# Kernel optimization log

Hardware: AMD Instinct MI355X
Metric: run time of the kernel (lower is better)

The kernel has to match this reference:

```python
import jax, jax.numpy as jnp
import numpy as np

EMBED = 512
HEADS = 8
HEAD_DIM = EMBED // HEADS


def setup_inputs() -> dict:
    key = jax.random.key(0)
    ks = jax.random.split(key, 8)
    N, S = 4, 2048
    values = jax.random.normal(ks[0], (N, S, EMBED), dtype=jnp.float32)
    keys = jax.random.normal(ks[1], (N, S, EMBED), dtype=jnp.float32)
    query = jax.random.normal(ks[2], (N, S, EMBED), dtype=jnp.float32)
    mask = jnp.ones((N, 1, 1, S), dtype=jnp.int32)
    # per-head projection weights (nn.Linear: y = x @ W.T), no bias
    Wv = jax.random.normal(ks[3], (HEAD_DIM, HEAD_DIM), dtype=jnp.float32) / np.sqrt(HEAD_DIM)
    Wk = jax.random.normal(ks[4], (HEAD_DIM, HEAD_DIM), dtype=jnp.float32) / np.sqrt(HEAD_DIM)
    Wq = jax.random.normal(ks[5], (HEAD_DIM, HEAD_DIM), dtype=jnp.float32) / np.sqrt(HEAD_DIM)
    Wo = jax.random.normal(ks[6], (EMBED, EMBED), dtype=jnp.float32) / np.sqrt(EMBED)
    bo = jax.random.normal(ks[7], (EMBED,), dtype=jnp.float32) * 0.01
    return {"values": values, "keys": keys, "query": query, "mask": mask,
            "Wv": Wv, "Wk": Wk, "Wq": Wq, "Wo": Wo, "bo": bo}


def reference(values, keys, query, mask, Wv, Wk, Wq, Wo, bo):
    N, S, _ = query.shape
    scale = jnp.sqrt(jnp.float32(HEAD_DIM))
    v = values.reshape(N, S, HEADS, HEAD_DIM) @ Wv.T
    k = keys.reshape(N, S, HEADS, HEAD_DIM) @ Wk.T
    q = query.reshape(N, S, HEADS, HEAD_DIM) @ Wq.T
    energy = jnp.einsum('nqhd,nkhd->nhqk', q, k) / scale  # [N,H,S,S]
    energy = jnp.where(mask == 0, jnp.float32(-1e20), energy)
    attn = jax.nn.softmax(energy, axis=3)
    # dropout is identity in eval mode
    out = jnp.einsum('nhql,nlhd->nqhd', attn, v).reshape(N, S, EMBED)
    return out @ Wo.T + bo
```

## Files before the change

kernel.cpp:

```cpp
#include <hip/hip_runtime.h>
#include <hip/hip_bf16.h>

#define EMB 512
#define NHEADS 8
#define HD 64
#define SEQ 2048

typedef float f32x4 __attribute__((ext_vector_type(4)));
typedef short short8 __attribute__((ext_vector_type(8)));
typedef unsigned short ushort4_t __attribute__((ext_vector_type(4)));

#define MFMA(a, b, c) __builtin_amdgcn_mfma_f32_16x16x32_bf16((a), (b), (c), 0, 0, 0)

__device__ inline unsigned short f2bf(float f) {
    union { float f; unsigned u; } v; v.f = f;
    unsigned r = v.u + 0x7fffu + ((v.u >> 16) & 1u);
    return (unsigned short)(r >> 16);
}

__device__ inline unsigned cvt_pk_bf16(float a, float b) {
    unsigned r;
    asm("v_cvt_pk_bf16_f32 %0, %1, %2" : "=v"(r) : "v"(a), "v"(b));
    return r;
}

__device__ inline short8 f8_to_bf8(float4 a, float4 b) {
    short8 r;
    r[0] = (short)f2bf(a.x); r[1] = (short)f2bf(a.y);
    r[2] = (short)f2bf(a.z); r[3] = (short)f2bf(a.w);
    r[4] = (short)f2bf(b.x); r[5] = (short)f2bf(b.y);
    r[6] = (short)f2bf(b.z); r[7] = (short)f2bf(b.w);
    return r;
}

__global__ __launch_bounds__(256) void qkv_proj_kernel(
    const float* __restrict__ vin, const float* __restrict__ kin,
    const float* __restrict__ qin, const unsigned short* __restrict__ wqkvb,
    unsigned short* __restrict__ q_ws, unsigned short* __restrict__ k_ws,
    unsigned short* __restrict__ vt_ws)
{
    const int z = blockIdx.y;
    const float* __restrict__ x = (z == 0) ? qin : (z == 1 ? kin : vin);
    const unsigned short* __restrict__ wb = wqkvb + z * HD * HD;

    const int bid = blockIdx.x;
    const int st = bid & 15;
    const int h  = (bid >> 4) & 7;
    const int n  = bid >> 7;

    const int lane = threadIdx.x & 63;
    const int w    = threadIdx.x >> 6;
    const int lo = lane & 15, hi = lane >> 4;
    const int s_base = st * 128 + w * 32;

    short8 b[2][4];
#pragma unroll
    for (int nb = 0; nb < 4; ++nb)
#pragma unroll
        for (int kb = 0; kb < 2; ++kb)
            b[kb][nb] = *(const short8*)(wb + (lo + 16 * nb) * HD + kb * 32 + hi * 8);

    short8 a[2][2];
#pragma unroll
    for (int sub = 0; sub < 2; ++sub) {
        const float* xr = x + ((size_t)n * SEQ + s_base + 16 * sub + lo) * EMB + h * HD;
#pragma unroll
        for (int kb = 0; kb < 2; ++kb) {
            const float4* p = (const float4*)(xr + kb * 32 + hi * 8);
            a[sub][kb] = f8_to_bf8(p[0], p[1]);
        }
    }

    f32x4 acc[2][4];
#pragma unroll
    for (int sub = 0; sub < 2; ++sub)
#pragma unroll
        for (int nb = 0; nb < 4; ++nb) {
            f32x4 t = {0.f, 0.f, 0.f, 0.f};
            t = MFMA(a[sub][0], b[0][nb], t);
            t = MFMA(a[sub][1], b[1][nb], t);
            acc[sub][nb] = t;
        }

    const size_t nh = (size_t)n * NHEADS + h;
    if (z < 2) {
        const float sc = (z == 0) ? 0.18033688011112042f : 1.0f;
        unsigned short* o = (z == 0 ? q_ws : k_ws) + nh * SEQ * HD;
#pragma unroll
        for (int sub = 0; sub < 2; ++sub)
#pragma unroll
            for (int nb = 0; nb < 4; ++nb)
#pragma unroll
                for (int i = 0; i < 4; ++i)
                    o[(size_t)(s_base + 16 * sub + hi * 4 + i) * HD + lo + 16 * nb] =
                        f2bf(acc[sub][nb][i] * sc);
    } else {
        unsigned short* o = vt_ws + nh * HD * SEQ;
#pragma unroll
        for (int sub = 0; sub < 2; ++sub)
#pragma unroll
            for (int nb = 0; nb < 4; ++nb) {
                ushort4_t pk;
                pk[0] = f2bf(acc[sub][nb][0]); pk[1] = f2bf(acc[sub][nb][1]);
                pk[2] = f2bf(acc[sub][nb][2]); pk[3] = f2bf(acc[sub][nb][3]);
                *(ushort4_t*)(o + (size_t)(lo + 16 * nb) * SEQ + s_base + 16 * sub + hi * 4) = pk;
            }
    }
}

__global__ __launch_bounds__(256) void wconv_kernel(
    const float* __restrict__ Wo, unsigned short* __restrict__ wob)
{
    const int idx = (blockIdx.x * 256 + threadIdx.x) * 8;
    const float4* p = (const float4*)(Wo + idx);
    short8 r = f8_to_bf8(p[0], p[1]);
    *(short8*)(wob + idx) = r;
}

__global__ __launch_bounds__(256) void wqkvconv_kernel(
    const float* __restrict__ Wq, const float* __restrict__ Wk,
    const float* __restrict__ Wv, unsigned short* __restrict__ wqkvb)
{
    const int idx = (blockIdx.x * 256 + threadIdx.x) * 8;
    const float* src = (idx < 4096) ? (Wq + idx)
                     : (idx < 8192) ? (Wk + idx - 4096)
                                    : (Wv + idx - 8192);
    const float4* p = (const float4*)src;
    short8 r = f8_to_bf8(p[0], p[1]);
    *(short8*)(wqkvb + idx) = r;
}

__global__ __launch_bounds__(64) void maskflags_kernel(
    const int* __restrict__ mask, unsigned* __restrict__ flags)
{
    const int n = blockIdx.x;
    const int t = threadIdx.x;
    bool has0 = false;
    if (t < 32) {
        const int* mrow = mask + (size_t)n * SEQ + t * 64;
#pragma unroll 4
        for (int j = 0; j < 64; j += 4) {
            int4 m4 = *(const int4*)(mrow + j);
            has0 |= (m4.x == 0) | (m4.y == 0) | (m4.z == 0) | (m4.w == 0);
        }
    }
    unsigned long long b = __ballot(has0);
    if (t == 0) flags[n] = (unsigned)(b & 0xffffffffu);
}

__global__ __launch_bounds__(512, 2) void attn_kernel(
    const unsigned short* __restrict__ q_ws, const unsigned short* __restrict__ k_ws,
    const unsigned short* __restrict__ vt_ws, const int* __restrict__ mask,
    const unsigned* __restrict__ flags, unsigned short* __restrict__ ao_ws)
{
    __shared__ __align__(16) unsigned short klds[64][72];
    __shared__ __align__(16) unsigned short vlds[64][72];
    __shared__ __align__(16) int            mlds[64];
    __shared__ __align__(16) unsigned short plds[8][2][16][72];

    const int tid  = threadIdx.x;
    const int lane = tid & 63;
    const int w    = tid >> 6;
    const int lo = lane & 15, hi = lane >> 4;
    const int bid = (blockIdx.x & 7) * 32 + (blockIdx.x >> 3);
    const int wid = bid * 8 + w;
    const int qt2 = wid & 63;
    const int h   = (wid >> 6) & 7;
    const int n   = wid >> 9;
    const size_t nh = (size_t)n * NHEADS + h;

    const unsigned short* qp = q_ws + nh * SEQ * HD;
    const unsigned short* kp = k_ws + nh * SEQ * HD;
    const unsigned short* vp = vt_ws + nh * HD * SEQ;
    const int* mp = mask + (size_t)n * SEQ;
    const unsigned fl = flags[n];

    const int q0 = qt2 * 32;
    short8 aq[2][2];
#pragma unroll
    for (int qi = 0; qi < 2; ++qi)
#pragma unroll
        for (int kb = 0; kb < 2; ++kb)
            aq[qi][kb] = *(const short8*)(qp + (size_t)(q0 + 16 * qi + lo) * HD
                                          + kb * 32 + hi * 8);

    f32x4 o[2][4];
    float lacc[2] = {0.f, 0.f};
#pragma unroll
    for (int qi = 0; qi < 2; ++qi)
#pragma unroll
        for (int nb = 0; nb < 4; ++nb)
            o[qi][nb] = (f32x4){0.f, 0.f, 0.f, 0.f};

    const int sr = tid >> 3;
    const int sc = (tid & 7) * 8;

    short8 rk = *(const short8*)(kp + (size_t)sr * HD + sc);
    short8 rv = *(const short8*)(vp + (size_t)sr * SEQ + sc);
    int    rm = (w == 0) ? mp[lane] : 0;

    for (int t = 0; t < 32; ++t) {
        const int kt = t * 64;
        __syncthreads();
        *(short8*)(&klds[sr][sc]) = rk;
        *(short8*)(&vlds[sr][sc]) = rv;
        if (w == 0) mlds[lane] = rm;
        __syncthreads();

        if (t < 31) {
            const int ktn = kt + 64;
            rk = *(const short8*)(kp + (size_t)(ktn + sr) * HD + sc);
            rv = *(const short8*)(vp + (size_t)sr * SEQ + ktn + sc);
            rm = (w == 0) ? mp[ktn + lane] : 0;
        }

        short8 k0[4], k1[4], va0[4], va1[4];
#pragma unroll
        for (int nb = 0; nb < 4; ++nb) {
            k0[nb]  = *(const short8*)(&klds[16 * nb + lo][hi * 8]);
            k1[nb]  = *(const short8*)(&klds[16 * nb + lo][32 + hi * 8]);
            va0[nb] = *(const short8*)(&vlds[16 * nb + lo][hi * 8]);
            va1[nb] = *(const short8*)(&vlds[16 * nb + lo][32 + hi * 8]);
        }
        const bool masked = (fl >> t) & 1u;
#pragma unroll
        for (int qi = 0; qi < 2; ++qi) {
            f32x4 e[4];
#pragma unroll
            for (int nb = 0; nb < 4; ++nb) {
                f32x4 tt = {0.f, 0.f, 0.f, 0.f};
                tt = MFMA(k0[nb], aq[qi][0], tt);
                tt = MFMA(k1[nb], aq[qi][1], tt);
                e[nb] = tt;
            }
            if (masked) {
#pragma unroll
                for (int nb = 0; nb < 4; ++nb) {
                    const int4 mm = *(const int4*)(&mlds[16 * nb + 4 * hi]);
                    if (mm.x == 0) e[nb][0] = -1e30f;
                    if (mm.y == 0) e[nb][1] = -1e30f;
                    if (mm.z == 0) e[nb][2] = -1e30f;
                    if (mm.w == 0) e[nb][3] = -1e30f;
                }
            }
#pragma unroll
            for (int nb = 0; nb < 4; ++nb) {
                float p0 = __builtin_amdgcn_exp2f(e[nb][0]);
                float p1 = __builtin_amdgcn_exp2f(e[nb][1]);
                float p2 = __builtin_amdgcn_exp2f(e[nb][2]);
                float p3 = __builtin_amdgcn_exp2f(e[nb][3]);
                lacc[qi] += (p0 + p1) + (p2 + p3);
                uint2 pk;
                pk.x = cvt_pk_bf16(p0, p1);
                pk.y = cvt_pk_bf16(p2, p3);
                *(uint2*)(&plds[w][qi][lo][16 * nb + 4 * hi]) = pk;
            }
            short8 pa0 = *(const short8*)(&plds[w][qi][lo][hi * 8]);
            short8 pa1 = *(const short8*)(&plds[w][qi][lo][32 + hi * 8]);
#pragma unroll
            for (int nb = 0; nb < 4; ++nb) {
                o[qi][nb] = MFMA(va0[nb], pa0, o[qi][nb]);
                o[qi][nb] = MFMA(va1[nb], pa1, o[qi][nb]);
            }
        }
    }

#pragma unroll
    for (int qi = 0; qi < 2; ++qi) {
        lacc[qi] += __shfl_xor(lacc[qi], 16);
        lacc[qi] += __shfl_xor(lacc[qi], 32);
        const float linv = 1.0f / lacc[qi];
        unsigned short* op = ao_ws + ((size_t)n * SEQ + q0 + 16 * qi + lo) * EMB + h * HD;
#pragma unroll
        for (int nb = 0; nb < 4; ++nb) {
            ushort4_t pk;
            pk[0] = f2bf(o[qi][nb][0] * linv);
            pk[1] = f2bf(o[qi][nb][1] * linv);
            pk[2] = f2bf(o[qi][nb][2] * linv);
            pk[3] = f2bf(o[qi][nb][3] * linv);
            *(ushort4_t*)(op + 16 * nb + 4 * hi) = pk;
        }
    }
}

__global__ __launch_bounds__(256) void out_proj_kernel(
    const unsigned short* __restrict__ ao_ws, const unsigned short* __restrict__ wob,
    const float* __restrict__ bo, float* __restrict__ out)
{
    const int bid = blockIdx.x;
    const int nc = bid & 7;
    const int mt = bid >> 3;
    const int lane = threadIdx.x & 63;
    const int w = threadIdx.x >> 6;
    const int lo = lane & 15, hi = lane >> 4;
    const int m0 = mt * 128 + w * 32;
    const int e0 = nc * 64;

    f32x4 acc[2][4];
#pragma unroll
    for (int sub = 0; sub < 2; ++sub)
#pragma unroll
        for (int nb = 0; nb < 4; ++nb)
            acc[sub][nb] = (f32x4){0.f, 0.f, 0.f, 0.f};

    const unsigned short* ar0 = ao_ws + (size_t)(m0 + lo) * EMB;
    const unsigned short* ar1 = ao_ws + (size_t)(m0 + 16 + lo) * EMB;
    for (int k0 = 0; k0 < EMB; k0 += 32) {
        short8 a0 = *(const short8*)(ar0 + k0 + hi * 8);
        short8 a1 = *(const short8*)(ar1 + k0 + hi * 8);
#pragma unroll
        for (int nb = 0; nb < 4; ++nb) {
            short8 b = *(const short8*)(wob + (size_t)(e0 + lo + 16 * nb) * EMB + k0 + hi * 8);
            acc[0][nb] = MFMA(a0, b, acc[0][nb]);
            acc[1][nb] = MFMA(a1, b, acc[1][nb]);
        }
    }
#pragma unroll
    for (int sub = 0; sub < 2; ++sub)
#pragma unroll
        for (int nb = 0; nb < 4; ++nb) {
            float bias = bo[e0 + lo + 16 * nb];
#pragma unroll
            for (int i = 0; i < 4; ++i)
                out[(size_t)(m0 + 16 * sub + hi * 4 + i) * EMB + e0 + lo + 16 * nb] =
                    acc[sub][nb][i] + bias;
        }
}

extern "C" void kernel_launch(void* const* d_in, const int* in_sizes, int n_in,
                              void* d_out, int out_size, void* d_ws, size_t ws_size,
                              hipStream_t stream)
{
    const float* vin = (const float*)d_in[0];
    const float* kin = (const float*)d_in[1];
    const float* qin = (const float*)d_in[2];
    const int*  mask = (const int*)d_in[3];
    const float* Wv  = (const float*)d_in[4];
    const float* Wk  = (const float*)d_in[5];
    const float* Wq  = (const float*)d_in[6];
    const float* Wo  = (const float*)d_in[7];
    const float* bo  = (const float*)d_in[8];
    float* out = (float*)d_out;

    const int N = in_sizes[0] / (SEQ * EMB);

    char* ws = (char*)d_ws;
    const size_t qkv_bytes = (size_t)N * NHEADS * SEQ * HD * 2;
    unsigned short* q_ws  = (unsigned short*)(ws);
    unsigned short* k_ws  = (unsigned short*)(ws + qkv_bytes);
    unsigned short* vt_ws = (unsigned short*)(ws + 2 * qkv_bytes);
    unsigned short* ao_ws = (unsigned short*)(ws + 3 * qkv_bytes);
    unsigned short* wob   = (unsigned short*)(ws + 4 * qkv_bytes);
    unsigned*       flags = (unsigned*)(ws + 4 * qkv_bytes + (size_t)EMB * EMB * 2);
    unsigned short* wqkvb = (unsigned short*)(ws + 4 * qkv_bytes + (size_t)EMB * EMB * 2 + 4096);

    hipLaunchKernelGGL(wconv_kernel, dim3(EMB * EMB / 2048), dim3(256), 0, stream,
                       Wo, wob);
    hipLaunchKernelGGL(wqkvconv_kernel, dim3(6), dim3(256), 0, stream,
                       Wq, Wk, Wv, wqkvb);
    hipLaunchKernelGGL(maskflags_kernel, dim3(N), dim3(64), 0, stream,
                       mask, flags);
    hipLaunchKernelGGL(qkv_proj_kernel, dim3(N * NHEADS * (SEQ / 128), 3), dim3(256), 0, stream,
                       vin, kin, qin, wqkvb, q_ws, k_ws, vt_ws);
    hipLaunchKernelGGL(attn_kernel, dim3(N * NHEADS * (SEQ / 32) / 8), dim3(512), 0, stream,
                       q_ws, k_ws, vt_ws, mask, flags, ao_ws);
    hipLaunchKernelGGL(out_proj_kernel, dim3((N * SEQ / 128) * (EMB / 64)), dim3(256), 0, stream,
                       ao_ws, wob, bo, out);
}
```

Before: 108.2 us.

## Switch attention to 32x32x16 MFMA and keep P in registers via permlane32 swap

The attention inner loop moves from 16x16x32 MFMA tiles to 32x32x16 MFMA tiles, so each wave handles its 32 query rows with larger matrix instructions. The softmax probabilities no longer go through a per-wave LDS staging buffer. They are repacked in registers with v_permlane32_swap so they can serve directly as the A operand of the PV MFMA. This removes the LDS write, read and wait for P. In exchange the launch bounds drop to one block per SIMD group, the output is written with scalar 2-byte stores, and the row normalisers now pass through LDS.

Result: faster. 95.61 us (-11.6%).

```diff
diff --git a/kernel.cpp b/kernel.cpp
--- a/kernel.cpp
+++ b/kernel.cpp
@@ -7,10 +7,13 @@
 #define SEQ 2048
 
 typedef float f32x4 __attribute__((ext_vector_type(4)));
+typedef float f32x16 __attribute__((ext_vector_type(16)));
 typedef short short8 __attribute__((ext_vector_type(8)));
 typedef unsigned short ushort4_t __attribute__((ext_vector_type(4)));
-
-#define MFMA(a, b, c) __builtin_amdgcn_mfma_f32_16x16x32_bf16((a), (b), (c), 0, 0, 0)
+typedef unsigned uint2v __attribute__((ext_vector_type(2)));
+
+#define MFMA(a, b, c)   __builtin_amdgcn_mfma_f32_16x16x32_bf16((a), (b), (c), 0, 0, 0)
+#define MFMA32(a, b, c) __builtin_amdgcn_mfma_f32_32x32x16_bf16((a), (b), (c), 0, 0, 0)
 
 __device__ inline unsigned short f2bf(float f) {
     union { float f; unsigned u; } v; v.f = f;
@@ -22,6 +25,21 @@
     unsigned r;
     asm("v_cvt_pk_bf16_f32 %0, %1, %2" : "=v"(r) : "v"(a), "v"(b));
     return r;
+}
+
+__device__ inline void plswap(unsigned &a, unsigned &b) {
+#if __has_builtin(__builtin_amdgcn_permlane32_swap)
+    uint2v r = __builtin_amdgcn_permlane32_swap(a, b, false, false);
+    a = r[0]; b = r[1];
+#else
+    asm volatile("v_permlane32_swap_b32 %0, %1" : "+v"(a), "+v"(b));
+#endif
+}
+
+__device__ inline short8 mk8(unsigned a, unsigned b, unsigned c, unsigned d) {
+    union { unsigned u[4]; short8 s; } x;
+    x.u[0] = a; x.u[1] = b; x.u[2] = c; x.u[3] = d;
+    return x.s;
 }
 
 __device__ inline short8 f8_to_bf8(float4 a, float4 b) {
@@ -148,7 +166,7 @@
     if (t == 0) flags[n] = (unsigned)(b & 0xffffffffu);
 }
 
-__global__ __launch_bounds__(512, 2) void attn_kernel(
+__global__ __launch_bounds__(512, 1) void attn_kernel(
     const unsigned short* __restrict__ q_ws, const unsigned short* __restrict__ k_ws,
     const unsigned short* __restrict__ vt_ws, const int* __restrict__ mask,
     const unsigned* __restrict__ flags, unsigned short* __restrict__ ao_ws)
@@ -156,15 +174,16 @@
     __shared__ __align__(16) unsigned short klds[64][72];
     __shared__ __align__(16) unsigned short vlds[64][72];
     __shared__ __align__(16) int            mlds[64];
-    __shared__ __align__(16) unsigned short plds[8][2][16][72];
+    __shared__ __align__(16) float          llds[8][32];
 
     const int tid  = threadIdx.x;
     const int lane = tid & 63;
     const int w    = tid >> 6;
-    const int lo = lane & 15, hi = lane >> 4;
+    const int l31  = lane & 31;
+    const int hi5  = lane >> 5;
     const int bid = (blockIdx.x & 7) * 32 + (blockIdx.x >> 3);
     const int wid = bid * 8 + w;
-    const int qt2 = wid & 63;
+    const int qb  = wid & 63;
     const int h   = (wid >> 6) & 7;
     const int n   = wid >> 9;
     const size_t nh = (size_t)n * NHEADS + h;
@@ -175,26 +194,19 @@
     const int* mp = mask + (size_t)n * SEQ;
     const unsigned fl = flags[n];
 
-    const int q0 = qt2 * 32;
-    short8 aq[2][2];
-#pragma unroll
-    for (int qi = 0; qi < 2; ++qi)
-#pragma unroll
-        for (int kb = 0; kb < 2; ++kb)
-            aq[qi][kb] = *(const short8*)(qp + (size_t)(q0 + 16 * qi + lo) * HD
-                                          + kb * 32 + hi * 8);
-
-    f32x4 o[2][4];
-    float lacc[2] = {0.f, 0.f};
-#pragma unroll
-    for (int qi = 0; qi < 2; ++qi)
-#pragma unroll
-        for (int nb = 0; nb < 4; ++nb)
-            o[qi][nb] = (f32x4){0.f, 0.f, 0.f, 0.f};
+    const int q0 = qb * 32;
+    short8 bq[4];
+#pragma unroll
+    for (int s = 0; s < 4; ++s)
+        bq[s] = *(const short8*)(qp + (size_t)(q0 + l31) * HD + 16 * s + 8 * hi5);
+
+    f32x16 o0, o1;
+#pragma unroll
+    for (int r = 0; r < 16; ++r) { o0[r] = 0.f; o1[r] = 0.f; }
+    float lacc = 0.f;
 
     const int sr = tid >> 3;
     const int sc = (tid & 7) * 8;
-
     short8 rk = *(const short8*)(kp + (size_t)sr * HD + sc);
     short8 rv = *(const short8*)(vp + (size_t)sr * SEQ + sc);
     int    rm = (w == 0) ? mp[lane] : 0;
@@ -214,72 +226,57 @@
             rm = (w == 0) ? mp[ktn + lane] : 0;
         }
 
-        short8 k0[4], k1[4], va0[4], va1[4];
-#pragma unroll
-        for (int nb = 0; nb < 4; ++nb) {
-            k0[nb]  = *(const short8*)(&klds[16 * nb + lo][hi * 8]);
-            k1[nb]  = *(const short8*)(&klds[16 * nb + lo][32 + hi * 8]);
-            va0[nb] = *(const short8*)(&vlds[16 * nb + lo][hi * 8]);
-            va1[nb] = *(const short8*)(&vlds[16 * nb + lo][32 + hi * 8]);
-        }
         const bool masked = (fl >> t) & 1u;
-#pragma unroll
-        for (int qi = 0; qi < 2; ++qi) {
-            f32x4 e[4];
-#pragma unroll
-            for (int nb = 0; nb < 4; ++nb) {
-                f32x4 tt = {0.f, 0.f, 0.f, 0.f};
-                tt = MFMA(k0[nb], aq[qi][0], tt);
-                tt = MFMA(k1[nb], aq[qi][1], tt);
-                e[nb] = tt;
+        short8 pa[4];
+#pragma unroll
+        for (int kb = 0; kb < 2; ++kb) {
+            f32x16 e;
+#pragma unroll
+            for (int r = 0; r < 16; ++r) e[r] = 0.f;
+#pragma unroll
+            for (int s = 0; s < 4; ++s) {
+                short8 ak = *(const short8*)(&klds[32 * kb + l31][16 * s + 8 * hi5]);
+                e = MFMA32(ak, bq[s], e);
             }
             if (masked) {
 #pragma unroll
-                for (int nb = 0; nb < 4; ++nb) {
-                    const int4 mm = *(const int4*)(&mlds[16 * nb + 4 * hi]);
-                    if (mm.x == 0) e[nb][0] = -1e30f;
-                    if (mm.y == 0) e[nb][1] = -1e30f;
-                    if (mm.z == 0) e[nb][2] = -1e30f;
-                    if (mm.w == 0) e[nb][3] = -1e30f;
+                for (int r = 0; r < 16; ++r) {
+                    const int key = 32 * kb + (r & 3) + 8 * (r >> 2) + 4 * hi5;
+                    if (mlds[key] == 0) e[r] = -1e30f;
                 }
             }
-#pragma unroll
-            for (int nb = 0; nb < 4; ++nb) {
-                float p0 = __builtin_amdgcn_exp2f(e[nb][0]);
-                float p1 = __builtin_amdgcn_exp2f(e[nb][1]);
-                float p2 = __builtin_amdgcn_exp2f(e[nb][2]);
-                float p3 = __builtin_amdgcn_exp2f(e[nb][3]);
-                lacc[qi] += (p0 + p1) + (p2 + p3);
-                uint2 pk;
-                pk.x = cvt_pk_bf16(p0, p1);
-                pk.y = cvt_pk_bf16(p2, p3);
-                *(uint2*)(&plds[w][qi][lo][16 * nb + 4 * hi]) = pk;
+            unsigned wv[8];
+#pragma unroll
+            for (int r2 = 0; r2 < 8; ++r2) {
+                float p0 = __builtin_amdgcn_exp2f(e[2 * r2]);
+                float p1 = __builtin_amdgcn_exp2f(e[2 * r2 + 1]);
+                lacc += p0 + p1;
+                wv[r2] = cvt_pk_bf16(p0, p1);
             }
-            short8 pa0 = *(const short8*)(&plds[w][qi][lo][hi * 8]);
-            short8 pa1 = *(const short8*)(&plds[w][qi][lo][32 + hi * 8]);
-#pragma unroll
-            for (int nb = 0; nb < 4; ++nb) {
-                o[qi][nb] = MFMA(va0[nb], pa0, o[qi][nb]);
-                o[qi][nb] = MFMA(va1[nb], pa1, o[qi][nb]);
-            }
-        }
-    }
-
-#pragma unroll
-    for (int qi = 0; qi < 2; ++qi) {
-        lacc[qi] += __shfl_xor(lacc[qi], 16);
-        lacc[qi] += __shfl_xor(lacc[qi], 32);
-        const float linv = 1.0f / lacc[qi];
-        unsigned short* op = ao_ws + ((size_t)n * SEQ + q0 + 16 * qi + lo) * EMB + h * HD;
-#pragma unroll
-        for (int nb = 0; nb < 4; ++nb) {
-            ushort4_t pk;
-            pk[0] = f2bf(o[qi][nb][0] * linv);
-            pk[1] = f2bf(o[qi][nb][1] * linv);
-            pk[2] = f2bf(o[qi][nb][2] * linv);
-            pk[3] = f2bf(o[qi][nb][3] * linv);
-            *(ushort4_t*)(op + 16 * nb + 4 * hi) = pk;
-        }
+            plswap(wv[0], wv[2]); plswap(wv[1], wv[3]);
+            plswap(wv[4], wv[6]); plswap(wv[5], wv[7]);
+            pa[2 * kb]     = mk8(wv[0], wv[1], wv[2], wv[3]);
+            pa[2 * kb + 1] = mk8(wv[4], wv[5], wv[6], wv[7]);
+        }
+#pragma unroll
+        for (int s = 0; s < 4; ++s) {
+            short8 bv0 = *(const short8*)(&vlds[l31][16 * s + 8 * hi5]);
+            short8 bv1 = *(const short8*)(&vlds[32 + l31][16 * s + 8 * hi5]);
+            o0 = MFMA32(pa[s], bv0, o0);
+            o1 = MFMA32(pa[s], bv1, o1);
+        }
+    }
+
+    lacc += __shfl_xor(lacc, 32);
+    if (lane < 32) llds[w][lane] = 1.0f / lacc;
+
+    unsigned short* op = ao_ws + ((size_t)n * SEQ + q0) * EMB + h * HD;
+#pragma unroll
+    for (int r = 0; r < 16; ++r) {
+        const int qrow = (r & 3) + 8 * (r >> 2) + 4 * hi5;
+        const float linv = llds[w][qrow];
+        op[(size_t)qrow * EMB + l31]      = f2bf(o0[r] * linv);
+        op[(size_t)qrow * EMB + 32 + l31] = f2bf(o1[r] * linv);
     }
 }
 
```
